# Performance work log

Measured on AMD Instinct MI355X. Metric: run time of the kernel, lower is better.

The kernel has to match this reference:

```python
import jax, jax.numpy as jnp
import numpy as np

N_NODES = 50000
N_EDGES = 800000
IN_DIM = 128
OUT_DIM = 64
NEG_SLOPE = 0.01  # torch F.leaky_relu default


def setup_inputs() -> dict:
    key = jax.random.key(0)
    k1, k2, k3, k4, k5 = jax.random.split(key, 5)
    features = jax.random.normal(k1, (N_NODES, IN_DIM), dtype=jnp.float32)
    # xavier-ish scale for weights
    fc_w = jax.random.normal(k2, (OUT_DIM, IN_DIM), dtype=jnp.float32) * (1.0 / np.sqrt(IN_DIM))
    attn_w = jax.random.normal(k3, (2 * OUT_DIM,), dtype=jnp.float32) * (1.0 / np.sqrt(2 * OUT_DIM))
    src = jax.random.randint(k4, (N_EDGES,), 0, N_NODES, dtype=jnp.int32)
    dst = jax.random.randint(k5, (N_EDGES,), 0, N_NODES, dtype=jnp.int32)
    return {"features": features, "fc_w": fc_w, "attn_w": attn_w, "src": src, "dst": dst}


def reference(features, fc_w, attn_w, src, dst):
    n = features.shape[0]
    out_dim = fc_w.shape[0]
    # z = fc(features), [N, out_dim]
    z = features @ fc_w.T
    # attn_fc([z_src || z_dst]) = z_src @ w_src + z_dst @ w_dst
    a_src = z @ attn_w[:out_dim]   # [N]
    a_dst = z @ attn_w[out_dim:]   # [N]
    e = a_src[src] + a_dst[dst]    # [E] per-edge raw score
    e = jnp.where(e > 0, e, NEG_SLOPE * e)  # leaky_relu
    # edge softmax over incoming edges of each dst node
    e_max = jax.ops.segment_max(e, dst, num_segments=n)      # [N]
    w = jnp.exp(e - e_max[dst])                               # [E]
    denom = jax.ops.segment_sum(w, dst, num_segments=n)       # [N]
    # weighted neighbor sum: sum_e alpha_e * z[src_e]
    num = jax.ops.segment_sum(w[:, None] * z[src], dst, num_segments=n)  # [N, out_dim]
    h = num / jnp.where(denom > 0, denom, 1.0)[:, None]
    # activation = elu
    h = jax.nn.elu(h)
    return h
```

## Files before the change

kernel.cpp:

```cpp
#include <hip/hip_runtime.h>
#include <hip/hip_bf16.h>
#include <hip/hip_fp16.h>

#define N_NODES 50000
#define N_EDGES 800000
#define IN_DIM 128
#define OUT_DIM 64
#define NEG_SLOPE 0.01f

#define N_STRIPS (N_NODES / 16)
#define Z_BLOCKS ((N_STRIPS + 3) / 4)
#define E_I4 (N_EDGES / 4)

#define NB4 ((N_NODES + 31) / 32)
#define CAP4 1024
#define EB 100
#define CHUNK_I4 (E_I4 / EB)

typedef __bf16 bf16x8 __attribute__((ext_vector_type(8)));
typedef float f32x4 __attribute__((ext_vector_type(4)));

__device__ __forceinline__ unsigned short f2bf_us(float f) {
  __hip_bfloat16 h = __float2bfloat16(f);
  return *reinterpret_cast<unsigned short*>(&h);
}
__device__ __forceinline__ bf16x8 pack_bf16(float4 lo, float4 hi) {
  union { bf16x8 v; unsigned short u[8]; } r;
  r.u[0] = f2bf_us(lo.x); r.u[1] = f2bf_us(lo.y);
  r.u[2] = f2bf_us(lo.z); r.u[3] = f2bf_us(lo.w);
  r.u[4] = f2bf_us(hi.x); r.u[5] = f2bf_us(hi.y);
  r.u[6] = f2bf_us(hi.z); r.u[7] = f2bf_us(hi.w);
  return r.v;
}
__device__ __forceinline__ float bflo(unsigned u) {
  return __uint_as_float(u << 16);
}
__device__ __forceinline__ float bfhi(unsigned u) {
  return __uint_as_float(u & 0xffff0000u);
}

__global__ __launch_bounds__(256) void gat_z_hist(
    const float* __restrict__ feat, const float* __restrict__ fcw,
    const float* __restrict__ attnw, __hip_bfloat16* __restrict__ z,
    float* __restrict__ asrc, float* __restrict__ adst,
    const int* __restrict__ dst, int* __restrict__ hist_g) {
  if (blockIdx.x >= Z_BLOCKS) {
    __shared__ int hist[NB4];
    const int tid = threadIdx.x;
    const int bb = blockIdx.x - Z_BLOCKS;
    const int i0 = bb * CHUNK_I4;
    for (int i = tid; i < NB4; i += 256) hist[i] = 0;
    __syncthreads();
    for (int t = i0 + tid; t < i0 + CHUNK_I4; t += 256) {
      const int4 d = ((const int4*)dst)[t];
      atomicAdd(&hist[d.x >> 5], 1);
      atomicAdd(&hist[d.y >> 5], 1);
      atomicAdd(&hist[d.z >> 5], 1);
      atomicAdd(&hist[d.w >> 5], 1);
    }
    __syncthreads();
    int* row = hist_g + (size_t)bb * NB4;
    for (int i = tid; i < NB4; i += 256) row[i] = hist[i];
    return;
  }

  const int lane = threadIdx.x & 63;
  const int m = lane & 15;
  const int quad = lane >> 4;
  const int wv = blockIdx.x * 4 + (threadIdx.x >> 6);
  if (wv >= N_STRIPS) return;
  const int n0 = wv * 16;

  bf16x8 bfrag[4][4];
#pragma unroll
  for (int t = 0; t < 4; ++t) {
    const float* wr = fcw + (size_t)(m + 16 * t) * IN_DIM + quad * 8;
#pragma unroll
    for (int c = 0; c < 4; ++c) {
      float4 lo = *(const float4*)(wr + c * 32);
      float4 hi = *(const float4*)(wr + c * 32 + 4);
      bfrag[t][c] = pack_bf16(lo, hi);
    }
  }

  f32x4 acc[4] = {{0.f, 0.f, 0.f, 0.f}, {0.f, 0.f, 0.f, 0.f},
                  {0.f, 0.f, 0.f, 0.f}, {0.f, 0.f, 0.f, 0.f}};
  const float* ar = feat + (size_t)(n0 + m) * IN_DIM + quad * 8;
#pragma unroll
  for (int c = 0; c < 4; ++c) {
    float4 lo = *(const float4*)(ar + c * 32);
    float4 hi = *(const float4*)(ar + c * 32 + 4);
    const bf16x8 af = pack_bf16(lo, hi);
#pragma unroll
    for (int t = 0; t < 4; ++t)
      acc[t] = __builtin_amdgcn_mfma_f32_16x16x32_bf16(af, bfrag[t][c],
                                                       acc[t], 0, 0, 0);
  }

#pragma unroll
  for (int t = 0; t < 4; ++t)
#pragma unroll
    for (int r = 0; r < 4; ++r)
      z[(size_t)(n0 + quad * 4 + r) * OUT_DIM + m + 16 * t] =
          __float2bfloat16(acc[t][r]);

  float aws[4], awd[4];
#pragma unroll
  for (int t = 0; t < 4; ++t) {
    aws[t] = attnw[m + 16 * t];
    awd[t] = attnw[OUT_DIM + m + 16 * t];
  }
  float ps[4], pd[4];
#pragma unroll
  for (int r = 0; r < 4; ++r) {
    float s = 0.f, d = 0.f;
#pragma unroll
    for (int t = 0; t < 4; ++t) {
      s = fmaf(acc[t][r], aws[t], s);
      d = fmaf(acc[t][r], awd[t], d);
    }
    ps[r] = s;
    pd[r] = d;
  }
#pragma unroll
  for (int off = 1; off < 16; off <<= 1) {
#pragma unroll
    for (int r = 0; r < 4; ++r) {
      ps[r] += __shfl_xor(ps[r], off, 64);
      pd[r] += __shfl_xor(pd[r], off, 64);
    }
  }
  if (m == 0) {
#pragma unroll
    for (int r = 0; r < 4; ++r) {
      asrc[n0 + quad * 4 + r] = ps[r];
      adst[n0 + quad * 4 + r] = pd[r];
    }
  }
}

__global__ __launch_bounds__(512) void gat_scan(
    const int* __restrict__ hist_g, int* __restrict__ hoff,
    int* __restrict__ cnt) {
  const int nb = blockIdx.x * 512 + threadIdx.x;
  if (nb >= NB4) return;
  int run = 0;
  for (int eb = 0; eb < EB; ++eb) {
    const int v = hist_g[(size_t)eb * NB4 + nb];
    hoff[(size_t)eb * NB4 + nb] = run;
    run += v;
  }
  cnt[nb] = run;
}

__global__ __launch_bounds__(1024) void gat_scatter_w(
    const float* __restrict__ asrc, const float* __restrict__ adst,
    const int* __restrict__ src, const int* __restrict__ dst,
    const int* __restrict__ hoff, unsigned long long* __restrict__ pairs) {
  __shared__ int cur[NB4];
  const int tid = threadIdx.x;
  const int bb = blockIdx.x;
  const int i0 = bb * CHUNK_I4;
  const int* hrow = hoff + (size_t)bb * NB4;
  for (int i = tid; i < NB4; i += 1024) cur[i] = hrow[i];
  __syncthreads();
  for (int t = i0 + tid; t < i0 + CHUNK_I4; t += 1024) {
    const int4 s = ((const int4*)src)[t];
    const int4 d = ((const int4*)dst)[t];
#define BKT_PUT(dd, ss)                                                    \
  {                                                                        \
    const float a = asrc[ss] + adst[dd];                                   \
    const float e = a > 0.f ? a : NEG_SLOPE * a;                           \
    const float w = __expf(e);                                             \
    const int nb = (dd) >> 5;                                              \
    const int r = atomicAdd(&cur[nb], 1);                                  \
    if (r < CAP4)                                                          \
      pairs[((size_t)nb << 10) + r] =                                      \
          ((unsigned long long)__float_as_uint(w) << 32) |                 \
          (unsigned)((((dd) & 31) << 16) | (ss));                          \
  }
    BKT_PUT(d.x, s.x)
    BKT_PUT(d.y, s.y)
    BKT_PUT(d.z, s.z)
    BKT_PUT(d.w, s.w)
#undef BKT_PUT
  }
}

__global__ __launch_bounds__(512) void gat_agg(
    const unsigned long long* __restrict__ pairs, const int* __restrict__ cnt,
    const __hip_bfloat16* __restrict__ zb, float* __restrict__ out) {
  __shared__ int hist[32];
  __shared__ int noff[33];
  __shared__ int cur[32];
  __shared__ float lw[CAP4];
  __shared__ int ls[CAP4];
  const int tid = threadIdx.x;
  const int b = blockIdx.x;
  const int c = min(cnt[b], CAP4);
  const unsigned long long* __restrict__ bp = pairs + ((size_t)b << 10);

  if (tid < 32) hist[tid] = 0;
  __syncthreads();
  for (int i = tid; i < c; i += 512)
    atomicAdd(&hist[((const unsigned*)bp)[2 * i] >> 16], 1);
  __syncthreads();
  if (tid < 32) {
    const int h = hist[tid];
    int s = h;
#pragma unroll
    for (int off = 1; off < 32; off <<= 1) {
      const int u = __shfl_up(s, off, 64);
      if (tid >= off) s += u;
    }
    noff[tid] = s - h;
    cur[tid] = s - h;
    if (tid == 31) noff[32] = s;
  }
  __syncthreads();
  for (int i = tid; i < c; i += 512) {
    const unsigned long long e = bp[i];
    const unsigned meta = (unsigned)e;
    const int r = atomicAdd(&cur[meta >> 16], 1);
    lw[r] = __uint_as_float((unsigned)(e >> 32));
    ls[r] = (int)(meta & 0xFFFFu);
  }
  __syncthreads();

  const int lane = tid & 63;
  const int wv = tid >> 6;
  const int g = lane >> 4;
  const int sl = lane & 15;
  const int j2 = sl & 3;
  const int eg = sl >> 2;

  const int ln = wv * 4 + g;
  const int node = b * 32 + ln;
  if (node >= N_NODES) return;

  const uint4* __restrict__ zp4 = (const uint4*)zb;
  const int o0 = noff[ln];
  const int o1 = noff[ln + 1];

  float acc[16];
#pragma unroll
  for (int cc = 0; cc < 16; ++cc) acc[cc] = 0.f;
  float dsum = 0.f;

  for (int i = o0 + eg; i < o1; i += 4) {
    const float w = lw[i];
    const int s = ls[i];
    dsum += w;
    const uint4 ua = zp4[(size_t)s * 8 + 2 * j2];
    const uint4 ub = zp4[(size_t)s * 8 + 2 * j2 + 1];
    acc[0] = fmaf(w, bflo(ua.x), acc[0]);
    acc[1] = fmaf(w, bfhi(ua.x), acc[1]);
    acc[2] = fmaf(w, bflo(ua.y), acc[2]);
    acc[3] = fmaf(w, bfhi(ua.y), acc[3]);
    acc[4] = fmaf(w, bflo(ua.z), acc[4]);
    acc[5] = fmaf(w, bfhi(ua.z), acc[5]);
    acc[6] = fmaf(w, bflo(ua.w), acc[6]);
    acc[7] = fmaf(w, bfhi(ua.w), acc[7]);
    acc[8] = fmaf(w, bflo(ub.x), acc[8]);
    acc[9] = fmaf(w, bfhi(ub.x), acc[9]);
    acc[10] = fmaf(w, bflo(ub.y), acc[10]);
    acc[11] = fmaf(w, bfhi(ub.y), acc[11]);
    acc[12] = fmaf(w, bflo(ub.z), acc[12]);
    acc[13] = fmaf(w, bfhi(ub.z), acc[13]);
    acc[14] = fmaf(w, bflo(ub.w), acc[14]);
    acc[15] = fmaf(w, bfhi(ub.w), acc[15]);
  }

#pragma unroll
  for (int off = 4; off <= 8; off <<= 1) {
#pragma unroll
    for (int cc = 0; cc < 16; ++cc) acc[cc] += __shfl_xor(acc[cc], off, 64);
    dsum += __shfl_xor(dsum, off, 64);
  }

  if (eg == 0) {
    const float inv = 1.f / (dsum > 0.f ? dsum : 1.f);
    float4* __restrict__ orow = (float4*)(out + (size_t)node * OUT_DIM);
#pragma unroll
    for (int v = 0; v < 4; ++v) {
      float4 r;
      float h;
      h = acc[4 * v + 0] * inv; r.x = h > 0.f ? h : expm1f(h);
      h = acc[4 * v + 1] * inv; r.y = h > 0.f ? h : expm1f(h);
      h = acc[4 * v + 2] * inv; r.z = h > 0.f ? h : expm1f(h);
      h = acc[4 * v + 3] * inv; r.w = h > 0.f ? h : expm1f(h);
      orow[4 * j2 + v] = r;
    }
  }
}

extern "C" void kernel_launch(void* const* d_in, const int* in_sizes, int n_in,
                              void* d_out, int out_size, void* d_ws, size_t ws_size,
                              hipStream_t stream) {
  const float* feat  = (const float*)d_in[0];
  const float* fcw   = (const float*)d_in[1];
  const float* attnw = (const float*)d_in[2];
  const int* src     = (const int*)d_in[3];
  const int* dst     = (const int*)d_in[4];
  float* out = (float*)d_out;

  char* ws = (char*)d_ws;
  __hip_bfloat16* z = (__hip_bfloat16*)ws;
  ws += (size_t)N_NODES * OUT_DIM * sizeof(__hip_bfloat16);
  float* asrc = (float*)ws;   ws += (size_t)N_NODES * sizeof(float);
  float* adst = (float*)ws;   ws += (size_t)N_NODES * sizeof(float);
  int* hist_g = (int*)ws;     ws += (size_t)EB * NB4 * sizeof(int);
  int* hoff = (int*)ws;       ws += (size_t)EB * NB4 * sizeof(int);
  int* cnt = (int*)ws;        ws += (size_t)1568 * sizeof(int);
  unsigned long long* pairs = (unsigned long long*)ws;
  ws += (size_t)NB4 * CAP4 * sizeof(unsigned long long);

  gat_z_hist<<<Z_BLOCKS + EB, 256, 0, stream>>>(
      feat, fcw, attnw, z, asrc, adst, dst, hist_g);
  gat_scan<<<(NB4 + 511) / 512, 512, 0, stream>>>(hist_g, hoff, cnt);
  gat_scatter_w<<<EB, 1024, 0, stream>>>(asrc, adst, src, dst, hoff, pairs);
  gat_agg<<<NB4, 512, 0, stream>>>(pairs, cnt, z, out);
}
```

Before: 147.3 us.

## Move edge weight computation into aggregation and fuse scan with scatter

```diff
diff --git a/kernel.cpp b/kernel.cpp
--- a/kernel.cpp
+++ b/kernel.cpp
@@ -39,28 +39,62 @@
   return __uint_as_float(u & 0xffff0000u);
 }
 
-__global__ __launch_bounds__(256) void gat_z_hist(
+__global__ __launch_bounds__(256) void gat_hist(
+    const int* __restrict__ dst, int* __restrict__ hist_g) {
+  __shared__ int hist[NB4];
+  const int tid = threadIdx.x;
+  const int bb = blockIdx.x;
+  const int i0 = bb * CHUNK_I4;
+  for (int i = tid; i < NB4; i += 256) hist[i] = 0;
+  __syncthreads();
+  for (int t = i0 + tid; t < i0 + CHUNK_I4; t += 256) {
+    const int4 d = ((const int4*)dst)[t];
+    atomicAdd(&hist[d.x >> 5], 1);
+    atomicAdd(&hist[d.y >> 5], 1);
+    atomicAdd(&hist[d.z >> 5], 1);
+    atomicAdd(&hist[d.w >> 5], 1);
+  }
+  __syncthreads();
+  int* row = hist_g + (size_t)bb * NB4;
+  for (int i = tid; i < NB4; i += 256) row[i] = hist[i];
+}
+
+__global__ __launch_bounds__(256) void gat_z_scatter(
     const float* __restrict__ feat, const float* __restrict__ fcw,
     const float* __restrict__ attnw, __hip_bfloat16* __restrict__ z,
     float* __restrict__ asrc, float* __restrict__ adst,
-    const int* __restrict__ dst, int* __restrict__ hist_g) {
+    const int* __restrict__ src, const int* __restrict__ dst,
+    const int* __restrict__ hist_g, int* __restrict__ cnt,
+    unsigned* __restrict__ pairs) {
   if (blockIdx.x >= Z_BLOCKS) {
-    __shared__ int hist[NB4];
+    __shared__ int cur[NB4];
     const int tid = threadIdx.x;
     const int bb = blockIdx.x - Z_BLOCKS;
     const int i0 = bb * CHUNK_I4;
-    for (int i = tid; i < NB4; i += 256) hist[i] = 0;
+    for (int i = tid; i < NB4; i += 256) {
+      int run = 0;
+      for (int eb = 0; eb < bb; ++eb) run += hist_g[(size_t)eb * NB4 + i];
+      cur[i] = run;
+      if (bb == EB - 1) cnt[i] = run + hist_g[(size_t)(EB - 1) * NB4 + i];
+    }
     __syncthreads();
     for (int t = i0 + tid; t < i0 + CHUNK_I4; t += 256) {
+      const int4 s = ((const int4*)src)[t];
       const int4 d = ((const int4*)dst)[t];
-      atomicAdd(&hist[d.x >> 5], 1);
-      atomicAdd(&hist[d.y >> 5], 1);
-      atomicAdd(&hist[d.z >> 5], 1);
-      atomicAdd(&hist[d.w >> 5], 1);
-    }
-    __syncthreads();
-    int* row = hist_g + (size_t)bb * NB4;
-    for (int i = tid; i < NB4; i += 256) row[i] = hist[i];
+#define BKT_PUT(dd, ss)                                                    \
+  {                                                                        \
+    const int nb = (dd) >> 5;                                              \
+    const int r = atomicAdd(&cur[nb], 1);                                  \
+    if (r < CAP4)                                                          \
+      pairs[((size_t)nb << 10) + r] =                                      \
+          ((unsigned)((dd) & 31) << 16) | (unsigned)(ss);                  \
+  }
+      BKT_PUT(d.x, s.x)
+      BKT_PUT(d.y, s.y)
+      BKT_PUT(d.z, s.z)
+      BKT_PUT(d.w, s.w)
+#undef BKT_PUT
+    }
     return;
   }
 
@@ -139,71 +173,22 @@
   }
 }
 
-__global__ __launch_bounds__(512) void gat_scan(
-    const int* __restrict__ hist_g, int* __restrict__ hoff,
-    int* __restrict__ cnt) {
-  const int nb = blockIdx.x * 512 + threadIdx.x;
-  if (nb >= NB4) return;
-  int run = 0;
-  for (int eb = 0; eb < EB; ++eb) {
-    const int v = hist_g[(size_t)eb * NB4 + nb];
-    hoff[(size_t)eb * NB4 + nb] = run;
-    run += v;
-  }
-  cnt[nb] = run;
-}
-
-__global__ __launch_bounds__(1024) void gat_scatter_w(
-    const float* __restrict__ asrc, const float* __restrict__ adst,
-    const int* __restrict__ src, const int* __restrict__ dst,
-    const int* __restrict__ hoff, unsigned long long* __restrict__ pairs) {
-  __shared__ int cur[NB4];
-  const int tid = threadIdx.x;
-  const int bb = blockIdx.x;
-  const int i0 = bb * CHUNK_I4;
-  const int* hrow = hoff + (size_t)bb * NB4;
-  for (int i = tid; i < NB4; i += 1024) cur[i] = hrow[i];
-  __syncthreads();
-  for (int t = i0 + tid; t < i0 + CHUNK_I4; t += 1024) {
-    const int4 s = ((const int4*)src)[t];
-    const int4 d = ((const int4*)dst)[t];
-#define BKT_PUT(dd, ss)                                                    \
-  {                                                                        \
-    const float a = asrc[ss] + adst[dd];                                   \
-    const float e = a > 0.f ? a : NEG_SLOPE * a;                           \
-    const float w = __expf(e);                                             \
-    const int nb = (dd) >> 5;                                              \
-    const int r = atomicAdd(&cur[nb], 1);                                  \
-    if (r < CAP4)                                                          \
-      pairs[((size_t)nb << 10) + r] =                                      \
-          ((unsigned long long)__float_as_uint(w) << 32) |                 \
-          (unsigned)((((dd) & 31) << 16) | (ss));                          \
-  }
-    BKT_PUT(d.x, s.x)
-    BKT_PUT(d.y, s.y)
-    BKT_PUT(d.z, s.z)
-    BKT_PUT(d.w, s.w)
-#undef BKT_PUT
-  }
-}
-
 __global__ __launch_bounds__(512) void gat_agg(
-    const unsigned long long* __restrict__ pairs, const int* __restrict__ cnt,
-    const __hip_bfloat16* __restrict__ zb, float* __restrict__ out) {
+    const unsigned* __restrict__ pairs, const int* __restrict__ cnt,
+    const __hip_bfloat16* __restrict__ zb, const float* __restrict__ asrc,
+    const float* __restrict__ adst, float* __restrict__ out) {
   __shared__ int hist[32];
   __shared__ int noff[33];
   __shared__ int cur[32];
-  __shared__ float lw[CAP4];
-  __shared__ int ls[CAP4];
+  __shared__ int lsrc[CAP4];
   const int tid = threadIdx.x;
   const int b = blockIdx.x;
   const int c = min(cnt[b], CAP4);
-  const unsigned long long* __restrict__ bp = pairs + ((size_t)b << 10);
+  const unsigned* __restrict__ bp = pairs + ((size_t)b << 10);
 
   if (tid < 32) hist[tid] = 0;
   __syncthreads();
-  for (int i = tid; i < c; i += 512)
-    atomicAdd(&hist[((const unsigned*)bp)[2 * i] >> 16], 1);
+  for (int i = tid; i < c; i += 512) atomicAdd(&hist[bp[i] >> 16], 1);
   __syncthreads();
   if (tid < 32) {
     const int h = hist[tid];
@@ -219,11 +204,9 @@
   }
   __syncthreads();
   for (int i = tid; i < c; i += 512) {
-    const unsigned long long e = bp[i];
-    const unsigned meta = (unsigned)e;
-    const int r = atomicAdd(&cur[meta >> 16], 1);
-    lw[r] = __uint_as_float((unsigned)(e >> 32));
-    ls[r] = (int)(meta & 0xFFFFu);
+    const unsigned p = bp[i];
+    const int r = atomicAdd(&cur[p >> 16], 1);
+    lsrc[r] = (int)(p & 0xFFFFu);
   }
   __syncthreads();
 
@@ -241,6 +224,7 @@
   const uint4* __restrict__ zp4 = (const uint4*)zb;
   const int o0 = noff[ln];
   const int o1 = noff[ln + 1];
+  const float ad = adst[node];
 
   float acc[16];
 #pragma unroll
@@ -248,8 +232,10 @@
   float dsum = 0.f;
 
   for (int i = o0 + eg; i < o1; i += 4) {
-    const float w = lw[i];
-    const int s = ls[i];
+    const int s = lsrc[i];
+    const float a = asrc[s] + ad;
+    const float e = a > 0.f ? a : NEG_SLOPE * a;
+    const float w = __expf(e);
     dsum += w;
     const uint4 ua = zp4[(size_t)s * 8 + 2 * j2];
     const uint4 ub = zp4[(size_t)s * 8 + 2 * j2 + 1];
@@ -310,14 +296,12 @@
   float* asrc = (float*)ws;   ws += (size_t)N_NODES * sizeof(float);
   float* adst = (float*)ws;   ws += (size_t)N_NODES * sizeof(float);
   int* hist_g = (int*)ws;     ws += (size_t)EB * NB4 * sizeof(int);
-  int* hoff = (int*)ws;       ws += (size_t)EB * NB4 * sizeof(int);
   int* cnt = (int*)ws;        ws += (size_t)1568 * sizeof(int);
-  unsigned long long* pairs = (unsigned long long*)ws;
-  ws += (size_t)NB4 * CAP4 * sizeof(unsigned long long);
-
-  gat_z_hist<<<Z_BLOCKS + EB, 256, 0, stream>>>(
-      feat, fcw, attnw, z, asrc, adst, dst, hist_g);
-  gat_scan<<<(NB4 + 511) / 512, 512, 0, stream>>>(hist_g, hoff, cnt);
-  gat_scatter_w<<<EB, 1024, 0, stream>>>(asrc, adst, src, dst, hoff, pairs);
-  gat_agg<<<NB4, 512, 0, stream>>>(pairs, cnt, z, out);
-}
+  unsigned* pairs = (unsigned*)ws;
+  ws += (size_t)NB4 * CAP4 * sizeof(unsigned);
+
+  gat_hist<<<EB, 256, 0, stream>>>(dst, hist_g);
+  gat_z_scatter<<<Z_BLOCKS + EB, 256, 0, stream>>>(
+      feat, fcw, attnw, z, asrc, adst, src, dst, hist_g, cnt, pairs);
+  gat_agg<<<NB4, 512, 0, stream>>>(pairs, cnt, z, asrc, adst, out);
+}
```

Result: slower. 174.3 us (+18.4%).
